# Optimization experiments

Measured on AMD Instinct MI355X. Metric: run time of the kernel, lower is better.

Reference implementation:

```python
import jax, jax.numpy as jnp
import numpy as np
import math

C = 256          # in_channels
HEADS = 8
DQK = C // HEADS # 32
DV = C // HEADS  # 32
Q_STRIDE = 2
KV_STRIDE = 2
POS_DIM = C      # position_embedding_dim defaults to in_channels
WAVE = 1000.0


def _pos_embed(L_q, L_kv, q_stride, kv_stride):
    # sinusoidal relative-position embedding, (L_q, L_kv, POS_DIM//2)
    q_idx = jnp.arange(L_q, dtype=jnp.float32) * q_stride
    kv_idx = jnp.arange(L_kv, dtype=jnp.float32) * kv_stride
    diff = q_idx[:, None] - kv_idx[None, :]                      # position_magnitude=1
    feat_range = jnp.arange(POS_DIM // 4, dtype=jnp.float32)
    dim_mat = WAVE ** ((4.0 / POS_DIM) * feat_range)             # (POS_DIM//4,)
    ang = diff[:, :, None] / dim_mat                             # (L_q, L_kv, POS_DIM//4)
    return jnp.concatenate([jnp.sin(ang), jnp.cos(ang)], axis=-1)


def setup_inputs() -> dict:
    key = jax.random.key(0)
    ks = jax.random.split(key, 9)
    x = jax.random.normal(ks[0], (2, C, 96, 96), dtype=jnp.float32)
    s_c = 1.0 / math.sqrt(C)
    s_p = 1.0 / math.sqrt(POS_DIM // 2)
    Wq = jax.random.normal(ks[1], (C, C), dtype=jnp.float32) * s_c      # query_conv 1x1, no bias
    Wk = jax.random.normal(ks[2], (C, C), dtype=jnp.float32) * s_c      # key_conv 1x1
    Wv = jax.random.normal(ks[3], (C, C), dtype=jnp.float32) * s_c      # value_conv 1x1
    Wgx = jax.random.normal(ks[4], (C, POS_DIM // 2), dtype=jnp.float32) * s_p  # appr_geom_fc_x
    Wgy = jax.random.normal(ks[5], (C, POS_DIM // 2), dtype=jnp.float32) * s_p  # appr_geom_fc_y
    stdv = 1.0 / math.sqrt(DQK * 2)
    appr_bias = jax.random.uniform(ks[6], (C,), dtype=jnp.float32, minval=-stdv, maxval=stdv)
    Wproj = jax.random.normal(ks[7], (C, C), dtype=jnp.float32) * s_c   # proj_conv 1x1 (bias)
    bproj = jnp.zeros((C,), dtype=jnp.float32)
    gamma = jnp.array(0.5, dtype=jnp.float32)  # torch init is 0; nonzero so attn path matters
    return {"x": x, "Wq": Wq, "Wk": Wk, "Wv": Wv, "Wgx": Wgx, "Wgy": Wgy,
            "appr_bias": appr_bias, "Wproj": Wproj, "bproj": bproj, "gamma": gamma}


def reference(x, Wq, Wk, Wv, Wgx, Wgy, appr_bias, Wproj, bproj, gamma):
    n, c, H, W = x.shape
    # AvgPool2d(kernel_size=1, stride=s) == strided subsample
    x_q = x[:, :, ::Q_STRIDE, ::Q_STRIDE]
    x_kv = x[:, :, ::KV_STRIDE, ::KV_STRIDE]
    h, w = x_q.shape[2], x_q.shape[3]
    hk, wk = x_kv.shape[2], x_kv.shape[3]

    # 1x1 convs as channel matmuls -> (n, heads, d, h, w)
    q = jnp.einsum('oc,nchw->nohw', Wq, x_q).reshape(n, HEADS, DQK, h, w)
    k = jnp.einsum('oc,nchw->nohw', Wk, x_kv).reshape(n, HEADS, DQK, hk, wk)
    v = jnp.einsum('oc,nchw->nohw', Wv, x_kv).reshape(n, HEADS, DV, hk, wk)

    # relative-position features, scaled by 1/sqrt(2)
    emb_x = _pos_embed(w, wk, Q_STRIDE, KV_STRIDE)   # (w, wk, POS_DIM//2)
    emb_y = _pos_embed(h, hk, Q_STRIDE, KV_STRIDE)   # (h, hk, POS_DIM//2)
    inv_s2 = 1.0 / math.sqrt(2.0)
    pfx = (jnp.einsum('wve,oe->wvo', emb_x, Wgx).reshape(w, wk, HEADS, DQK)
           .transpose(2, 0, 1, 3)) * inv_s2          # (heads, w, wk, d)
    pfy = (jnp.einsum('hue,oe->huo', emb_y, Wgy).reshape(h, hk, HEADS, DQK)
           .transpose(2, 0, 1, 3)) * inv_s2          # (heads, h, hk, d)

    # attention_type '0110': bias-appr + appr-position terms
    ab = appr_bias.reshape(HEADS, DQK)
    e_bias = jnp.einsum('id,niduv->niuv', ab, k)               # (n,i,hk,wk)
    e_x = jnp.einsum('nidhw,iwvd->nihwv', q, pfx)              # (n,i,h,w,wk)
    e_y = jnp.einsum('nidhw,ihud->nihwu', q, pfy)              # (n,i,h,w,hk)

    energy = (e_bias[:, :, None, None, :, :]
              + e_y[:, :, :, :, :, None]
              + e_x[:, :, :, :, None, :])                       # (n,i,h,w,hk,wk)
    energy = energy.reshape(n, HEADS, h * w, hk * wk)
    attn = jax.nn.softmax(energy, axis=3)

    v2 = v.reshape(n, HEADS, DV, hk * wk)
    out = jnp.einsum('nisk,nidk->nids', attn, v2)              # (n,i,DV,h*w)
    out = out.reshape(n, HEADS * DV, h, w)
    out = jnp.einsum('oc,nchw->nohw', Wproj, out) + bproj[None, :, None, None]
    # q_downsample used -> bilinear upsample back (align_corners=False semantics)
    out = jax.image.resize(out, (n, c, H, W), method='bilinear')
    return gamma * out + x
```

## Files before the change

### kernel.cpp

```cpp
#include <hip/hip_runtime.h>
#include <math.h>

#define CC 256
#define HEADS 8
#define DD 32
#define GG 48
#define LL (GG*GG)
#define NB 2
#define PTAB_N 95

typedef float f32x4 __attribute__((ext_vector_type(4)));
typedef _Float16 f16x8 __attribute__((ext_vector_type(8)));
typedef _Float16 f16x4 __attribute__((ext_vector_type(4)));

#define OFF_XS   0
#define SZ_XS    (NB*CC*LL)
#define OFF_VBT  OFF_XS
#define OFF_EBT  (OFF_XS + 786432)
#define OFF_QB   (OFF_XS + SZ_XS)
#define SZ_QB    (NB*LL*CC)
#define OFF_PO   OFF_QB
#define OFF_VT   (OFF_QB + SZ_QB)
#define SZ_VT_F  (NB*CC*LL/2)
#define OFF_AO   (OFF_VT + SZ_VT_F)
#define OFF_XH   OFF_AO
#define SZ_AO    (NB*LL*CC)
#define OFF_EB   (OFF_AO + SZ_AO)
#define SZ_EB    (NB*HEADS*LL)
#define OFF_PTX  (OFF_EB + SZ_EB)
#define SZ_PT    (PTAB_N*CC)
#define OFF_PTY  (OFF_PTX + SZ_PT)
#define OFF_WB   (OFF_PTY + SZ_PT)

__global__ void k_xin(const float* __restrict__ x, _Float16* __restrict__ xh) {
    const int n = blockIdx.z, c0 = blockIdx.y*64, s0 = blockIdx.x*64;
    const int t = threadIdx.x;
    __shared__ _Float16 ldt[64*72];
    #pragma unroll
    for (int l = 0; l < 4; ++l) {
        int idx = t + 256*l;
        int cl = idx >> 4, s4 = idx & 15;
        const float* xb = x + (size_t)(n*CC + c0+cl)*96*96;
        #pragma unroll
        for (int e = 0; e < 4; ++e) {
            int s = s0 + s4*4 + e;
            int h = s / GG, w = s % GG;
            ldt[(s4*4+e)*72 + cl] = (_Float16)xb[(2*h)*96 + 2*w];
        }
    }
    __syncthreads();
    #pragma unroll
    for (int l = 0; l < 2; ++l) {
        int idx = t + 256*l;
        int sl = idx >> 3, jg = idx & 7;
        f16x8 o = *(const f16x8*)(ldt + sl*72 + jg*8);
        int s = s0 + sl;
        int p = ((c0 >> 3) + jg) ^ (s & 7);
        *(f16x8*)(xh + (size_t)(n*LL + s)*CC + p*8) = o;
    }
}

__global__ void k_prep(const float* __restrict__ Wgx, const float* __restrict__ Wgy,
                       const float* __restrict__ Wk, const float* __restrict__ ab,
                       float* __restrict__ ptx, float* __restrict__ pty,
                       float* __restrict__ wb) {
    const int which = blockIdx.y;
    const int t = threadIdx.x;
    if (which == 2) {
        int i = blockIdx.x;
        if (i < HEADS) {
            float acc = 0.f;
            for (int d = 0; d < DD; ++d) acc += ab[i*DD+d] * Wk[(i*DD+d)*CC + t];
            wb[i*CC + t] = acc;
        }
        return;
    }
    __shared__ float emb[128];
    int ddv = blockIdx.x;
    float diff = 2.0f * (float)(ddv - 47);
    if (t < 64) {
        float dim = powf(1000.0f, (float)t / 64.0f);
        float ang = diff / dim;
        emb[t]      = sinf(ang);
        emb[t + 64] = cosf(ang);
    }
    __syncthreads();
    const float* Wg = which ? Wgy : Wgx;
    float* pt = which ? pty : ptx;
    float acc = 0.f;
    #pragma unroll 8
    for (int e = 0; e < 128; ++e) acc += emb[e] * Wg[t*128 + e];
    pt[ddv*CC + t] = acc * 0.70710678118654752f;
}

__global__ __launch_bounds__(256) void k_gemm_qv(const float* __restrict__ Wq,
                                                 const float* __restrict__ Wv,
                                                 const float* __restrict__ wb,
                                                 const _Float16* __restrict__ xh,
                                                 float* __restrict__ qb,
                                                 _Float16* __restrict__ vtb,
                                                 float* __restrict__ ebx) {
    const int n  = blockIdx.z;
    const int my = blockIdx.y;
    const int j0 = blockIdx.x * 64;
    const int t = threadIdx.x;
    const int lane = t & 63, mw = t >> 6;
    __shared__ alignas(16) _Float16 As[64*256];
    __shared__ alignas(16) _Float16 Bs[64*256];

    #pragma unroll
    for (int l = 0; l < 8; ++l) {
        int idx = t + 256*l;
        int m = idx >> 5, j = idx & 31;
        int row = my*64 + m;
        f16x8 h = {};
        if (row < 520) {
            const float* src = (row < 256) ? (Wq + (size_t)row*CC + j*8)
                             : (row < 512) ? (Wv + (size_t)(row-256)*CC + j*8)
                                           : (wb + (size_t)(row-512)*CC + j*8);
            float4 v0 = *(const float4*)(src);
            float4 v1 = *(const float4*)(src + 4);
            h[0]=(_Float16)v0.x; h[1]=(_Float16)v0.y;
            h[2]=(_Float16)v0.z; h[3]=(_Float16)v0.w;
            h[4]=(_Float16)v1.x; h[5]=(_Float16)v1.y;
            h[6]=(_Float16)v1.z; h[7]=(_Float16)v1.w;
        }
        *(f16x8*)(As + m*256 + ((j ^ (m&7))*8)) = h;
    }
    {
        const _Float16* src = xh + (size_t)(n*LL + j0)*CC + mw*4096 + lane*8;
        _Float16* dst = Bs + mw*4096;
        #pragma unroll
        for (int c = 0; c < 8; ++c)
            __builtin_amdgcn_global_load_lds(src + c*512, dst + c*512, 16, 0, 0);
    }
    __syncthreads();

    const int r = lane & 15, g = lane >> 4;
    f16x8 af[8];
    #pragma unroll
    for (int kk = 0; kk < 8; ++kk)
        af[kk] = *(const f16x8*)(As + (mw*16 + r)*256 + (((kk*4+g) ^ (r&7))*8));
    f32x4 acc0 = {}, acc1 = {}, acc2 = {}, acc3 = {};
    #pragma unroll
    for (int kk = 0; kk < 8; ++kk) {
        f16x8 b0 = *(const f16x8*)(Bs + (0*16 + r)*256 + (((kk*4+g) ^ (r&7))*8));
        f16x8 b1 = *(const f16x8*)(Bs + (1*16 + r)*256 + (((kk*4+g) ^ (r&7))*8));
        f16x8 b2 = *(const f16x8*)(Bs + (2*16 + r)*256 + (((kk*4+g) ^ (r&7))*8));
        f16x8 b3 = *(const f16x8*)(Bs + (3*16 + r)*256 + (((kk*4+g) ^ (r&7))*8));
        acc0 = __builtin_amdgcn_mfma_f32_16x16x32_f16(af[kk], b0, acc0, 0,0,0);
        acc1 = __builtin_amdgcn_mfma_f32_16x16x32_f16(af[kk], b1, acc1, 0,0,0);
        acc2 = __builtin_amdgcn_mfma_f32_16x16x32_f16(af[kk], b2, acc2, 0,0,0);
        acc3 = __builtin_amdgcn_mfma_f32_16x16x32_f16(af[kk], b3, acc3, 0,0,0);
    }

    const int rowD = mw*16 + g*4;
    #pragma unroll
    for (int nf = 0; nf < 4; ++nf) {
        const f32x4& a = (nf==0)?acc0:(nf==1)?acc1:(nf==2)?acc2:acc3;
        int token = j0 + nf*16 + r;
        #pragma unroll
        for (int reg = 0; reg < 4; ++reg) {
            int row = my*64 + rowD + reg;
            float v = a[reg];
            if (my < 4) {
                qb[(size_t)(n*LL + token)*CC + row] = v;
            } else if (my < 8) {
                vtb[(size_t)(n*CC + row - 256)*LL + token] = (_Float16)v;
            } else {
                int i = row - 512;
                if (i < 8) ebx[(size_t)(n*HEADS + i)*LL + token] = __expf(v);
            }
        }
    }
}

__global__ void k_vtr(const _Float16* __restrict__ vtb, const float* __restrict__ ebx,
                      _Float16* __restrict__ vbT, _Float16* __restrict__ ebT) {
    const int ni = blockIdx.x;
    const int pair = blockIdx.y*256 + threadIdx.x;
    const int v = pair >> 5, d = pair & 31;
    const int sw = d & 7;
    const _Float16* vsrc = vtb + (size_t)(ni*32 + d)*LL;
    const float*  ebs  = ebx + (size_t)ni*LL;
    _Float16* dst = vbT + (size_t)ni*98304 + (size_t)(v*32 + d)*64;
    f16x8 z = {};
    #pragma unroll
    for (int c = 0; c < 6; ++c) {
        f16x8 o;
        #pragma unroll
        for (int e = 0; e < 8; ++e) {
            int u = c*8 + e;
            o[e] = (_Float16)((float)vsrc[u*48 + v] * ebs[u*48 + v]);
        }
        *(f16x8*)(dst + (c ^ sw)*8) = o;
    }
    *(f16x8*)(dst + (6 ^ sw)*8) = z;
    *(f16x8*)(dst + (7 ^ sw)*8) = z;
    if (d == 0) {
        _Float16* ed = ebT + (size_t)ni*3072 + (size_t)v*64;
        #pragma unroll
        for (int c = 0; c < 6; ++c) {
            f16x8 o;
            #pragma unroll
            for (int e = 0; e < 8; ++e)
                o[e] = (_Float16)ebs[(c*8+e)*48 + v];
            *(f16x8*)(ed + c*8) = o;
        }
        *(f16x8*)(ed + 48) = z;
        *(f16x8*)(ed + 56) = z;
    }
}

__global__ __launch_bounds__(256) void k_attn(const float* __restrict__ qb,
                                              const _Float16* __restrict__ vbT,
                                              const _Float16* __restrict__ ebT,
                                              const float* __restrict__ ptx,
                                              const float* __restrict__ pty,
                                              float* __restrict__ ao) {
    const int t = threadIdx.x;
    const int lane = t & 63;
    const int mw = t >> 6;
    const int ni = blockIdx.y;
    const int n = ni >> 3, i = ni & 7;
    const int s0 = blockIdx.x * 64;

    __shared__ alignas(16) char smpool[32768];
    float*    qs  = (float*)smpool;
    _Float16* pts = (_Float16*)(smpool + 8192);
    _Float16* Vt  = (_Float16*)smpool;
    __shared__ alignas(16) _Float16 Exs[64*56];
    __shared__ alignas(16) _Float16 Eys[64*72];

    #pragma unroll
    for (int l = 0; l < 2; ++l) {
        int f = t + 256*l;
        int r4 = f >> 3, dq = f & 7;
        float4 v4 = *(const float4*)(qb + (size_t)(n*LL + s0 + r4)*CC + i*32 + dq*4);
        *(float4*)(&qs[r4*32 + dq*4]) = v4;
    }
    for (int idx = t; idx < 2*PTAB_N*8; idx += 256) {
        int which = idx / (PTAB_N*8);
        int rem = idx % (PTAB_N*8);
        int ddv = rem >> 3, f4 = rem & 7;
        const float* src = (which ? ptx : pty) + (size_t)ddv*CC + i*32 + f4*4;
        float4 v = *(const float4*)src;
        f16x4 hh;
        hh[0]=(_Float16)v.x; hh[1]=(_Float16)v.y;
        hh[2]=(_Float16)v.z; hh[3]=(_Float16)v.w;
        *(f16x4*)(pts + which*(PTAB_N*40) + ddv*40 + f4*4) = hh;
    }
    __syncthreads();

    {
        const int rr = t >> 2, pp = t & 3;
        const int s = s0 + rr, h = s / GG, w = s % GG;
        float4 qreg[8];
        #pragma unroll
        for (int d4 = 0; d4 < 8; ++d4) qreg[d4] = *(const float4*)(qs + rr*32 + d4*4);
        float eyv[12], exv[12];
        float mey = -1e30f, mex = -1e30f;
        #pragma unroll
        for (int k = 0; k < 24; ++k) {
            int j = pp + 4*k;
            const _Float16* tp;
            if (k < 12) tp = pts + (h - j + 47)*40;
            else        tp = pts + PTAB_N*40 + (w - (j-48) + 47)*40;
            float acc = 0.f;
            #pragma unroll
            for (int d8 = 0; d8 < 4; ++d8) {
                f16x8 b = *(const f16x8*)(tp + d8*8);
                float4 a1v = qreg[2*d8], a2v = qreg[2*d8+1];
                acc += a1v.x*(float)b[0] + a1v.y*(float)b[1]
                     + a1v.z*(float)b[2] + a1v.w*(float)b[3]
                     + a2v.x*(float)b[4] + a2v.y*(float)b[5]
                     + a2v.z*(float)b[6] + a2v.w*(float)b[7];
            }
            if (k < 12) { eyv[k] = acc;    mey = fmaxf(mey, acc); }
            else        { exv[k-12] = acc; mex = fmaxf(mex, acc); }
        }
        mey = fmaxf(mey, __shfl_xor(mey, 1, 64));
        mey = fmaxf(mey, __shfl_xor(mey, 2, 64));
        mex = fmaxf(mex, __shfl_xor(mex, 1, 64));
        mex = fmaxf(mex, __shfl_xor(mex, 2, 64));
        #pragma unroll
        for (int k = 0; k < 12; ++k) {
            Eys[rr*72 + pp + 4*k] = (_Float16)__expf(eyv[k] - mey);
            Exs[rr*56 + pp + 4*k] = (_Float16)__expf(exv[k] - mex);
        }
    }
    for (int zi = t; zi < 64*16; zi += 256) {
        int r = zi >> 4, c = zi & 15;
        Eys[r*72 + 48 + c] = (_Float16)0.f;
    }
    __syncthreads();

    const int r = lane & 15, g = lane >> 4;
    const int rowA = mw*16 + r;
    const int rowD = mw*16 + g*4;

    f16x8 a0 = *(const f16x8*)(Eys + rowA*72 + g*8);
    f16x8 a1 = *(const f16x8*)(Eys + rowA*72 + 32 + g*8);

    const _Float16* vb = vbT + (size_t)ni*(48*32*64);
    const _Float16* et = ebT + (size_t)ni*(48*64);

    f32x4 hs0, hs1, hs2;
    {
        f32x4 zv = {0.f,0.f,0.f,0.f};
        f16x8 b0 = *(const f16x8*)(et + (0*16 + r)*64 + g*8);
        f16x8 b1 = *(const f16x8*)(et + (0*16 + r)*64 + 32 + g*8);
        hs0 = __builtin_amdgcn_mfma_f32_16x16x32_f16(a0, b0, zv, 0,0,0);
        hs0 = __builtin_amdgcn_mfma_f32_16x16x32_f16(a1, b1, hs0, 0,0,0);
        b0 = *(const f16x8*)(et + (1*16 + r)*64 + g*8);
        b1 = *(const f16x8*)(et + (1*16 + r)*64 + 32 + g*8);
        hs1 = __builtin_amdgcn_mfma_f32_16x16x32_f16(a0, b0, zv, 0,0,0);
        hs1 = __builtin_amdgcn_mfma_f32_16x16x32_f16(a1, b1, hs1, 0,0,0);
        b0 = *(const f16x8*)(et + (2*16 + r)*64 + g*8);
        b1 = *(const f16x8*)(et + (2*16 + r)*64 + 32 + g*8);
        hs2 = __builtin_amdgcn_mfma_f32_16x16x32_f16(a0, b0, zv, 0,0,0);
        hs2 = __builtin_amdgcn_mfma_f32_16x16x32_f16(a1, b1, hs2, 0,0,0);
    }
    float Sp[4];
    #pragma unroll
    for (int reg = 0; reg < 4; ++reg) {
        Sp[reg] = (float)Exs[(rowD+reg)*56 +  0 + r] * hs0[reg]
                + (float)Exs[(rowD+reg)*56 + 16 + r] * hs1[reg]
                + (float)Exs[(rowD+reg)*56 + 32 + r] * hs2[reg];
    }
    #pragma unroll
    for (int m = 1; m <= 8; m <<= 1) {
        #pragma unroll
        for (int reg = 0; reg < 4; ++reg)
            Sp[reg] += __shfl_xor(Sp[reg], m, 64);
    }

    #define STAGE(BUF, TT) { \
        const _Float16* src_ = vb + (size_t)(TT)*8192 + mw*2048 + lane*8; \
        _Float16* dst_ = Vt + (BUF)*8192 + mw*2048; \
        __builtin_amdgcn_global_load_lds(src_,        dst_,        16, 0, 0); \
        __builtin_amdgcn_global_load_lds(src_ + 512,  dst_ + 512,  16, 0, 0); \
        __builtin_amdgcn_global_load_lds(src_ + 1024, dst_ + 1024, 16, 0, 0); \
        __builtin_amdgcn_global_load_lds(src_ + 1536, dst_ + 1536, 16, 0, 0); }

    f32x4 oacc0 = {0.f,0.f,0.f,0.f}, oacc1 = {0.f,0.f,0.f,0.f};
    const int sw0 = (g ^ (r&7))*8;
    const int sw1 = ((g+4) ^ (r&7))*8;
    int buf = 0;
    STAGE(0, 0);
    __syncthreads();
    #pragma unroll 1
    for (int tt = 0; tt < 12; ++tt) {
        if (tt < 11) STAGE(buf^1, tt+1);
        const _Float16* VB = Vt + buf*8192;
        const int v0 = tt*4;
        f16x4 exh0 = *(const f16x4*)(Exs + (rowD+0)*56 + v0);
        f16x4 exh1 = *(const f16x4*)(Exs + (rowD+1)*56 + v0);
        f16x4 exh2 = *(const f16x4*)(Exs + (rowD+2)*56 + v0);
        f16x4 exh3 = *(const f16x4*)(Exs + (rowD+3)*56 + v0);
        #pragma unroll
        for (int q = 0; q < 8; ++q) {
            const int vl = q >> 1, dh = q & 1;
            const int row = vl*32 + dh*16 + r;
            f16x8 b0 = *(const f16x8*)(VB + row*64 + sw0);
            f16x8 b1 = *(const f16x8*)(VB + row*64 + sw1);
            float e0 = (float)exh0[vl];
            float e1 = (float)exh1[vl];
            float e2 = (float)exh2[vl];
            float e3 = (float)exh3[vl];
            f32x4 hz = {0.f,0.f,0.f,0.f};
            hz = __builtin_amdgcn_mfma_f32_16x16x32_f16(a0, b0, hz, 0,0,0);
            hz = __builtin_amdgcn_mfma_f32_16x16x32_f16(a1, b1, hz, 0,0,0);
            if (dh == 0) {
                oacc0[0] += e0*hz[0]; oacc0[1] += e1*hz[1];
                oacc0[2] += e2*hz[2]; oacc0[3] += e3*hz[3];
            } else {
                oacc1[0] += e0*hz[0]; oacc1[1] += e1*hz[1];
                oacc1[2] += e2*hz[2]; oacc1[3] += e3*hz[3];
            }
        }
        __syncthreads();
        buf ^= 1;
    }

    #pragma unroll
    for (int reg = 0; reg < 4; ++reg) {
        float inv = 1.0f / fmaxf(Sp[reg], 1e-30f);
        size_t base = (size_t)(n*LL + s0 + rowD + reg)*CC + i*32;
        ao[base + r]      = oacc0[reg] * inv;
        ao[base + 16 + r] = oacc1[reg] * inv;
    }
}

__global__ __launch_bounds__(256) void k_gemm_proj(const float* __restrict__ Wp,
                                                   const float* __restrict__ ao,
                                                   _Float16* __restrict__ po) {
    const int n  = blockIdx.z;
    const int m0 = blockIdx.y * 64;
    const int j0 = blockIdx.x * 64;
    const int t = threadIdx.x;
    const int lane = t & 63, mw = t >> 6;
    __shared__ alignas(16) _Float16 As[64*256];
    __shared__ alignas(16) _Float16 Bs[64*256];

    #pragma unroll
    for (int l = 0; l < 8; ++l) {
        int idx = t + 256*l;
        int m = idx >> 5, j = idx & 31;
        const float* srcA = Wp + (size_t)(m0 + m)*CC + j*8;
        float4 a0v = *(const float4*)srcA;
        float4 a1v = *(const float4*)(srcA + 4);
        f16x8 ha;
        ha[0]=(_Float16)a0v.x; ha[1]=(_Float16)a0v.y;
        ha[2]=(_Float16)a0v.z; ha[3]=(_Float16)a0v.w;
        ha[4]=(_Float16)a1v.x; ha[5]=(_Float16)a1v.y;
        ha[6]=(_Float16)a1v.z; ha[7]=(_Float16)a1v.w;
        *(f16x8*)(As + m*256 + ((j ^ (m&7))*8)) = ha;
        const float* srcB = ao + (size_t)(n*LL + j0 + m)*CC + j*8;
        float4 b0v = *(const float4*)srcB;
        float4 b1v = *(const float4*)(srcB + 4);
        f16x8 hb;
        hb[0]=(_Float16)b0v.x; hb[1]=(_Float16)b0v.y;
        hb[2]=(_Float16)b0v.z; hb[3]=(_Float16)b0v.w;
        hb[4]=(_Float16)b1v.x; hb[5]=(_Float16)b1v.y;
        hb[6]=(_Float16)b1v.z; hb[7]=(_Float16)b1v.w;
        *(f16x8*)(Bs + m*256 + ((j ^ (m&7))*8)) = hb;
    }
    __syncthreads();

    const int r = lane & 15, g = lane >> 4;
    f16x8 af[8];
    #pragma unroll
    for (int kk = 0; kk < 8; ++kk)
        af[kk] = *(const f16x8*)(As + (mw*16 + r)*256 + (((kk*4+g) ^ (r&7))*8));
    f32x4 acc0 = {}, acc1 = {}, acc2 = {}, acc3 = {};
    #pragma unroll
    for (int kk = 0; kk < 8; ++kk) {
        f16x8 b0 = *(const f16x8*)(Bs + (0*16 + r)*256 + (((kk*4+g) ^ (r&7))*8));
        f16x8 b1 = *(const f16x8*)(Bs + (1*16 + r)*256 + (((kk*4+g) ^ (r&7))*8));
        f16x8 b2 = *(const f16x8*)(Bs + (2*16 + r)*256 + (((kk*4+g) ^ (r&7))*8));
        f16x8 b3 = *(const f16x8*)(Bs + (3*16 + r)*256 + (((kk*4+g) ^ (r&7))*8));
        acc0 = __builtin_amdgcn_mfma_f32_16x16x32_f16(af[kk], b0, acc0, 0,0,0);
        acc1 = __builtin_amdgcn_mfma_f32_16x16x32_f16(af[kk], b1, acc1, 0,0,0);
        acc2 = __builtin_amdgcn_mfma_f32_16x16x32_f16(af[kk], b2, acc2, 0,0,0);
        acc3 = __builtin_amdgcn_mfma_f32_16x16x32_f16(af[kk], b3, acc3, 0,0,0);
    }

    const int rowD = mw*16 + g*4;
    #pragma unroll
    for (int nf = 0; nf < 4; ++nf) {
        const f32x4& a = (nf==0)?acc0:(nf==1)?acc1:(nf==2)?acc2:acc3;
        int token = j0 + nf*16 + r;
        #pragma unroll
        for (int reg = 0; reg < 4; ++reg) {
            int row = m0 + rowD + reg;
            po[(size_t)(n*CC + row)*LL + token] = (_Float16)a[reg];
        }
    }
}

__global__ void k_final(const float* __restrict__ x, const _Float16* __restrict__ po,
                        const float* __restrict__ bproj, const float* __restrict__ gammap,
                        float* __restrict__ out) {
    int idx = blockIdx.x*256 + threadIdx.x;
    if (idx >= NB*CC*96*96) return;
    int X = idx % 96, Y = (idx/96) % 96, o = (idx/(96*96)) % CC, n = idx/(96*96*CC);
    float gamma = gammap[0];
    float yf = Y*0.5f - 0.25f, xf = X*0.5f - 0.25f;
    float y0f = floorf(yf), x0f = floorf(xf);
    float tyy = yf - y0f, txx = xf - x0f;
    int y0 = (int)y0f, x0 = (int)x0f;
    int iy0 = max(y0,0), iy1 = min(y0+1,GG-1);
    int ix0 = max(x0,0), ix1 = min(x0+1,GG-1);
    const _Float16* pp = po + (size_t)(n*CC + o)*LL;
    float v00 = (float)pp[iy0*GG+ix0], v01 = (float)pp[iy0*GG+ix1];
    float v10 = (float)pp[iy1*GG+ix0], v11 = (float)pp[iy1*GG+ix1];
    float vy0 = v00 + txx*(v01-v00);
    float vy1 = v10 + txx*(v11-v10);
    float bil = vy0 + tyy*(vy1-vy0);
    out[idx] = gamma*(bil + bproj[o]) + x[idx];
}

extern "C" void kernel_launch(void* const* d_in, const int* in_sizes, int n_in,
                              void* d_out, int out_size, void* d_ws, size_t ws_size,
                              hipStream_t stream) {
    const float* x   = (const float*)d_in[0];
    const float* Wq  = (const float*)d_in[1];
    const float* Wk  = (const float*)d_in[2];
    const float* Wv  = (const float*)d_in[3];
    const float* Wgx = (const float*)d_in[4];
    const float* Wgy = (const float*)d_in[5];
    const float* ab  = (const float*)d_in[6];
    const float* Wp  = (const float*)d_in[7];
    const float* bp  = (const float*)d_in[8];
    const float* gm  = (const float*)d_in[9];
    float* ws = (float*)d_ws;
    _Float16* vbT = (_Float16*)(ws + OFF_VBT);
    _Float16* ebT = (_Float16*)(ws + OFF_EBT);
    float* qbp = ws + OFF_QB;
    _Float16* vtb = (_Float16*)(ws + OFF_VT);
    float* aop = ws + OFF_AO;
    _Float16* xh = (_Float16*)(ws + OFF_XH);
    float* ebp = ws + OFF_EB;
    float* ptxp= ws + OFF_PTX;
    float* ptyp= ws + OFF_PTY;
    float* wbp = ws + OFF_WB;
    _Float16* pop = (_Float16*)(ws + OFF_PO);
    float* out = (float*)d_out;

    k_xin<<<dim3(LL/64, CC/64, NB), 256, 0, stream>>>(x, xh);
    k_prep<<<dim3(PTAB_N, 3), 256, 0, stream>>>(Wgx, Wgy, Wk, ab, ptxp, ptyp, wbp);
    k_gemm_qv<<<dim3(LL/64, 9, NB), 256, 0, stream>>>(Wq, Wv, wbp, xh, qbp, vtb, ebp);
    k_vtr<<<dim3(NB*HEADS, 6), 256, 0, stream>>>(vtb, ebp, vbT, ebT);
    k_attn<<<dim3(LL/64, NB*HEADS), 256, 0, stream>>>(qbp, vbT, ebT, ptxp, ptyp, aop);
    k_gemm_proj<<<dim3(LL/64, 4, NB), 256, 0, stream>>>(Wp, aop, pop);
    k_final<<<(NB*CC*96*96 + 255)/256, 256, 0, stream>>>(x, pop, bp, gm, out);
}
```

Measured before the change: 81.68 us.

## Halve attention query tile and split value dims across waves

The attention kernel now handles 32 query rows per block instead of 64, so twice as many blocks launch. The four waves split into two row groups times two value-dimension halves, and each wave does half the MFMA work per V tile. This raises parallelism and shrinks LDS and registers per block. In exchange, each block stages the full V tiles and position tables for fewer queries, so global-to-LDS traffic per query doubles.

```diff
diff --git a/kernel.cpp b/kernel.cpp
--- a/kernel.cpp
+++ b/kernel.cpp
@@ -223,19 +223,17 @@
     const int mw = t >> 6;
     const int ni = blockIdx.y;
     const int n = ni >> 3, i = ni & 7;
-    const int s0 = blockIdx.x * 64;
+    const int s0 = blockIdx.x * 32;
 
     __shared__ alignas(16) char smpool[32768];
     float*    qs  = (float*)smpool;
-    _Float16* pts = (_Float16*)(smpool + 8192);
+    _Float16* pts = (_Float16*)(smpool + 4096);
     _Float16* Vt  = (_Float16*)smpool;
-    __shared__ alignas(16) _Float16 Exs[64*56];
-    __shared__ alignas(16) _Float16 Eys[64*72];
-
-    #pragma unroll
-    for (int l = 0; l < 2; ++l) {
-        int f = t + 256*l;
-        int r4 = f >> 3, dq = f & 7;
+    __shared__ alignas(16) _Float16 Exs[32*56];
+    __shared__ alignas(16) _Float16 Eys[32*72];
+
+    {
+        int r4 = t >> 3, dq = t & 7;
         float4 v4 = *(const float4*)(qb + (size_t)(n*LL + s0 + r4)*CC + i*32 + dq*4);
         *(float4*)(&qs[r4*32 + dq*4]) = v4;
     }
@@ -253,19 +251,19 @@
     __syncthreads();
 
     {
-        const int rr = t >> 2, pp = t & 3;
+        const int rr = t >> 3, pp = t & 7;
         const int s = s0 + rr, h = s / GG, w = s % GG;
         float4 qreg[8];
         #pragma unroll
         for (int d4 = 0; d4 < 8; ++d4) qreg[d4] = *(const float4*)(qs + rr*32 + d4*4);
-        float eyv[12], exv[12];
+        float eyv[6], exv[6];
         float mey = -1e30f, mex = -1e30f;
         #pragma unroll
-        for (int k = 0; k < 24; ++k) {
-            int j = pp + 4*k;
+        for (int k = 0; k < 12; ++k) {
+            int j = pp + 8*(k < 6 ? k : k-6);
             const _Float16* tp;
-            if (k < 12) tp = pts + (h - j + 47)*40;
-            else        tp = pts + PTAB_N*40 + (w - (j-48) + 47)*40;
+            if (k < 6) tp = pts + (h - j + 47)*40;
+            else       tp = pts + PTAB_N*40 + (w - j + 47)*40;
             float acc = 0.f;
             #pragma unroll
             for (int d8 = 0; d8 < 4; ++d8) {
@@ -276,28 +274,31 @@
                      + a2v.x*(float)b[4] + a2v.y*(float)b[5]
                      + a2v.z*(float)b[6] + a2v.w*(float)b[7];
             }
-            if (k < 12) { eyv[k] = acc;    mey = fmaxf(mey, acc); }
-            else        { exv[k-12] = acc; mex = fmaxf(mex, acc); }
+            if (k < 6) { eyv[k] = acc;   mey = fmaxf(mey, acc); }
+            else       { exv[k-6] = acc; mex = fmaxf(mex, acc); }
         }
         mey = fmaxf(mey, __shfl_xor(mey, 1, 64));
         mey = fmaxf(mey, __shfl_xor(mey, 2, 64));
+        mey = fmaxf(mey, __shfl_xor(mey, 4, 64));
         mex = fmaxf(mex, __shfl_xor(mex, 1, 64));
         mex = fmaxf(mex, __shfl_xor(mex, 2, 64));
-        #pragma unroll
-        for (int k = 0; k < 12; ++k) {
-            Eys[rr*72 + pp + 4*k] = (_Float16)__expf(eyv[k] - mey);
-            Exs[rr*56 + pp + 4*k] = (_Float16)__expf(exv[k] - mex);
-        }
-    }
-    for (int zi = t; zi < 64*16; zi += 256) {
+        mex = fmaxf(mex, __shfl_xor(mex, 4, 64));
+        #pragma unroll
+        for (int k = 0; k < 6; ++k) {
+            Eys[rr*72 + pp + 8*k] = (_Float16)__expf(eyv[k] - mey);
+            Exs[rr*56 + pp + 8*k] = (_Float16)__expf(exv[k] - mex);
+        }
+    }
+    for (int zi = t; zi < 32*16; zi += 256) {
         int r = zi >> 4, c = zi & 15;
         Eys[r*72 + 48 + c] = (_Float16)0.f;
     }
     __syncthreads();
 
     const int r = lane & 15, g = lane >> 4;
-    const int rowA = mw*16 + r;
-    const int rowD = mw*16 + g*4;
+    const int dh = mw >> 1;
+    const int rowA = (mw & 1)*16 + r;
+    const int rowD = (mw & 1)*16 + g*4;
 
     f16x8 a0 = *(const f16x8*)(Eys + rowA*72 + g*8);
     f16x8 a1 = *(const f16x8*)(Eys + rowA*72 + 32 + g*8);
@@ -343,7 +344,7 @@
         __builtin_amdgcn_global_load_lds(src_ + 1024, dst_ + 1024, 16, 0, 0); \
         __builtin_amdgcn_global_load_lds(src_ + 1536, dst_ + 1536, 16, 0, 0); }
 
-    f32x4 oacc0 = {0.f,0.f,0.f,0.f}, oacc1 = {0.f,0.f,0.f,0.f};
+    f32x4 oacc = {0.f,0.f,0.f,0.f};
     const int sw0 = (g ^ (r&7))*8;
     const int sw1 = ((g+4) ^ (r&7))*8;
     int buf = 0;
@@ -359,25 +360,17 @@
         f16x4 exh2 = *(const f16x4*)(Exs + (rowD+2)*56 + v0);
         f16x4 exh3 = *(const f16x4*)(Exs + (rowD+3)*56 + v0);
         #pragma unroll
-        for (int q = 0; q < 8; ++q) {
-            const int vl = q >> 1, dh = q & 1;
+        for (int vl = 0; vl < 4; ++vl) {
             const int row = vl*32 + dh*16 + r;
             f16x8 b0 = *(const f16x8*)(VB + row*64 + sw0);
             f16x8 b1 = *(const f16x8*)(VB + row*64 + sw1);
-            float e0 = (float)exh0[vl];
-            float e1 = (float)exh1[vl];
-            float e2 = (float)exh2[vl];
-            float e3 = (float)exh3[vl];
             f32x4 hz = {0.f,0.f,0.f,0.f};
             hz = __builtin_amdgcn_mfma_f32_16x16x32_f16(a0, b0, hz, 0,0,0);
             hz = __builtin_amdgcn_mfma_f32_16x16x32_f16(a1, b1, hz, 0,0,0);
-            if (dh == 0) {
-                oacc0[0] += e0*hz[0]; oacc0[1] += e1*hz[1];
-                oacc0[2] += e2*hz[2]; oacc0[3] += e3*hz[3];
-            } else {
-                oacc1[0] += e0*hz[0]; oacc1[1] += e1*hz[1];
-                oacc1[2] += e2*hz[2]; oacc1[3] += e3*hz[3];
-            }
+            oacc[0] += (float)exh0[vl]*hz[0];
+            oacc[1] += (float)exh1[vl]*hz[1];
+            oacc[2] += (float)exh2[vl]*hz[2];
+            oacc[3] += (float)exh3[vl]*hz[3];
         }
         __syncthreads();
         buf ^= 1;
@@ -387,8 +380,7 @@
     for (int reg = 0; reg < 4; ++reg) {
         float inv = 1.0f / fmaxf(Sp[reg], 1e-30f);
         size_t base = (size_t)(n*LL + s0 + rowD + reg)*CC + i*32;
-        ao[base + r]      = oacc0[reg] * inv;
-        ao[base + 16 + r] = oacc1[reg] * inv;
+        ao[base + dh*16 + r] = oacc[reg] * inv;
     }
 }
 
@@ -512,7 +504,7 @@
     k_prep<<<dim3(PTAB_N, 3), 256, 0, stream>>>(Wgx, Wgy, Wk, ab, ptxp, ptyp, wbp);
     k_gemm_qv<<<dim3(LL/64, 9, NB), 256, 0, stream>>>(Wq, Wv, wbp, xh, qbp, vtb, ebp);
     k_vtr<<<dim3(NB*HEADS, 6), 256, 0, stream>>>(vtb, ebp, vbT, ebT);
-    k_attn<<<dim3(LL/64, NB*HEADS), 256, 0, stream>>>(qbp, vbT, ebT, ptxp, ptyp, aop);
+    k_attn<<<dim3(LL/32, NB*HEADS), 256, 0, stream>>>(qbp, vbT, ebT, ptxp, ptyp, aop);
     k_gemm_proj<<<dim3(LL/64, 4, NB), 256, 0, stream>>>(Wp, aop, pop);
     k_final<<<(NB*CC*96*96 + 255)/256, 256, 0, stream>>>(x, pop, bp, gm, out);
 }
```

Result: slower. 86.76 us (median of 2 runs) (+6.2%).
